# Performance work log

Measured on AMD Instinct MI355X. Metric: run time of the kernel, lower is better.

Reference implementation:

```python
import jax, jax.numpy as jnp
import numpy as np

NBINS = 256

def _rescale_0_1(img):
    return (img + 1.0) * (127.0 / 255.0)

def _rescale_back(img):
    return img * (255.0 / 127.0) - 1.0

def _rgb_to_yuv_y(img):
    # tf.image.rgb_to_yuv luma coefficients; only Y channel is used downstream
    return img[..., 0] * 0.299 + img[..., 1] * 0.587 + img[..., 2] * 0.114

def _equalize_histogram(image):
    # tf.histogram_fixed_width over [0,1] with 256 bins (values clipped to range)
    idx = jnp.clip((image * NBINS).astype(jnp.int32), 0, NBINS - 1)
    hist = jnp.zeros((NBINS,), jnp.int32).at[idx.reshape(-1)].add(1)
    cdf = jnp.cumsum(hist)
    cdf_min = jnp.min(cdf)
    pix_cnt = image.shape[0] * image.shape[1]
    return (cdf - cdf_min).astype(jnp.float32) / jnp.float32(pix_cnt - 1)

def _interpolate(dx, dy, x):
    # brute-force searchsorted substitute: first index where dx - x > 0
    del_vals = dx[jnp.newaxis, :] - x[:, jnp.newaxis]          # [N, 256]
    ind_1 = jnp.argmax(jnp.sign(del_vals), axis=1)             # first positive
    ind_0 = jnp.clip(ind_1 - 1, 0, NBINS - 1)
    dx0, dx1 = dx[ind_0], dx[ind_1]
    dy0, dy1 = dy[ind_0], dy[ind_1]
    denom = dx1 - dx0
    safe_denom = jnp.where(denom == 0, jnp.float32(1.0), denom)
    interp = dy0 + (dy1 - dy0) * (x - dx0) / safe_denom
    return jnp.where(x <= dx[0], dy[0], jnp.where(x >= dx[-1], dy[-1], interp))

def setup_inputs() -> dict:
    key = jax.random.key(0)
    k1, k2 = jax.random.split(key)
    H, W = 1024, 1024
    src = jax.random.uniform(k1, (H, W, 3), jnp.float32, minval=-1.0, maxval=1.0)
    tgt = jax.random.uniform(k2, (H, W, 3), jnp.float32, minval=-1.0, maxval=1.0)
    return {"src": src, "tgt": tgt}

def reference(src, tgt):
    src = _rescale_0_1(src)
    tgt = _rescale_0_1(tgt)
    tgt_y = _rgb_to_yuv_y(tgt)
    h, w = src.shape[0], src.shape[1]
    floating_space = jnp.clip(jnp.arange(0.0, 1.00001, 1.0 / 255.0, dtype=jnp.float32), 0.0, 1.0)
    source = src[:, :, 0]
    cdfsrc = _equalize_histogram(source)
    cdftgt = _equalize_histogram(tgt_y)
    pxmap = _interpolate(cdftgt, floating_space, cdfsrc)
    pxmap = _interpolate(floating_space, pxmap, source.reshape(h * w))
    pxmap = pxmap.reshape(h, w, 1)
    res = jnp.clip(pxmap, 0.0, 1.0)
    return _rescale_back(res)
```

## Files before the change

kernel.cpp:

```cpp
#include <hip/hip_runtime.h>

#define NBINS 256
#define HBLK 512

__device__ __forceinline__ float fs_val(int j) {
    const float c = (float)(1.0 / 255.0);
    float v = (float)j * c;
    return v > 1.0f ? 1.0f : v;
}

__device__ __forceinline__ int bin_of(float s) {
    int i = (int)(s * 256.0f);
    i = i < 0 ? 0 : i;
    i = i > NBINS - 1 ? NBINS - 1 : i;
    return i;
}

__global__ void hm_hist(const float* __restrict__ src,
                        const float* __restrict__ tgt,
                        int* __restrict__ partS, int* __restrict__ partT,
                        int nquad) {
    __shared__ int hs[NBINS];
    __shared__ int ht[NBINS];
    for (int i = threadIdx.x; i < NBINS; i += blockDim.x) { hs[i] = 0; ht[i] = 0; }
    __syncthreads();

    const float c1 = (float)(127.0 / 255.0);
    int tid = blockIdx.x * blockDim.x + threadIdx.x;
    int stride = gridDim.x * blockDim.x;

    for (int q = tid; q < nquad; q += stride) {
        const float4* s4 = (const float4*)(src + 12 * (size_t)q);
        float4 a = s4[0], b = s4[1], c = s4[2];
        float p0 = (a.x + 1.0f) * c1;
        float p1 = (a.w + 1.0f) * c1;
        float p2 = (b.z + 1.0f) * c1;
        float p3 = (c.y + 1.0f) * c1;
        atomicAdd(&hs[bin_of(p0)], 1);
        atomicAdd(&hs[bin_of(p1)], 1);
        atomicAdd(&hs[bin_of(p2)], 1);
        atomicAdd(&hs[bin_of(p3)], 1);

        const float4* t4 = (const float4*)(tgt + 12 * (size_t)q);
        float4 ta = t4[0], tb = t4[1], tc = t4[2];
        {
            float r = (ta.x + 1.0f) * c1, g = (ta.y + 1.0f) * c1, bb = (ta.z + 1.0f) * c1;
            atomicAdd(&ht[bin_of(r * 0.299f + g * 0.587f + bb * 0.114f)], 1);
        }
        {
            float r = (ta.w + 1.0f) * c1, g = (tb.x + 1.0f) * c1, bb = (tb.y + 1.0f) * c1;
            atomicAdd(&ht[bin_of(r * 0.299f + g * 0.587f + bb * 0.114f)], 1);
        }
        {
            float r = (tb.z + 1.0f) * c1, g = (tb.w + 1.0f) * c1, bb = (tc.x + 1.0f) * c1;
            atomicAdd(&ht[bin_of(r * 0.299f + g * 0.587f + bb * 0.114f)], 1);
        }
        {
            float r = (tc.y + 1.0f) * c1, g = (tc.z + 1.0f) * c1, bb = (tc.w + 1.0f) * c1;
            atomicAdd(&ht[bin_of(r * 0.299f + g * 0.587f + bb * 0.114f)], 1);
        }
    }
    __syncthreads();
    for (int i = threadIdx.x; i < NBINS; i += blockDim.x) {
        partS[(size_t)blockIdx.x * NBINS + i] = hs[i];
        partT[(size_t)blockIdx.x * NBINS + i] = ht[i];
    }
}

__global__ void __launch_bounds__(1024)
hm_cdf_map(const int* __restrict__ partS,
           const int* __restrict__ partT,
           float* __restrict__ pxmap, int npix) {
    __shared__ int sS[NBINS];
    __shared__ int sT[NBINS];
    __shared__ float cdfT[NBINS];
    int t = threadIdx.x;
    int bin = t & (NBINS - 1);
    int split = t >> 8;

    if (t < NBINS) { sS[t] = 0; sT[t] = 0; }
    __syncthreads();

    int accS = 0, accT = 0;
    for (int b = split; b < HBLK; b += 4) {
        accS += partS[(size_t)b * NBINS + bin];
        accT += partT[(size_t)b * NBINS + bin];
    }
    atomicAdd(&sS[bin], accS);
    atomicAdd(&sT[bin], accT);
    __syncthreads();

    for (int off = 1; off < NBINS; off <<= 1) {
        int vS = 0, vT = 0, aS = 0, aT = 0;
        if (t < NBINS) {
            vS = sS[t]; vT = sT[t];
            if (t >= off) { aS = sS[t - off]; aT = sT[t - off]; }
        }
        __syncthreads();
        if (t < NBINS) { sS[t] = vS + aS; sT[t] = vT + aT; }
        __syncthreads();
    }

    if (t < NBINS) {
        int minS = sS[0], minT = sT[0];
        float denomN = (float)(npix - 1);
        float xS = (float)(sS[t] - minS) / denomN;
        cdfT[t] = (float)(sT[t] - minT) / denomN;
        __syncthreads();

        float res;
        if (xS <= cdfT[0]) {
            res = fs_val(0);
        } else if (xS >= cdfT[NBINS - 1]) {
            res = fs_val(NBINS - 1);
        } else {
            int lo = 0, hi = NBINS - 1;
            while (hi - lo > 1) {
                int mid = (lo + hi) >> 1;
                if (cdfT[mid] > xS) hi = mid; else lo = mid;
            }
            int j1 = hi, j0 = hi - 1;
            float dx0 = cdfT[j0], dx1 = cdfT[j1];
            float dy0 = fs_val(j0), dy1 = fs_val(j1);
            res = dy0 + (dy1 - dy0) * (xS - dx0) / (dx1 - dx0);
        }
        pxmap[t] = res;
    } else {
        __syncthreads();
    }
}

__global__ void hm_apply(const float* __restrict__ src,
                         const float* __restrict__ pxmap,
                         float* __restrict__ out, int nquad) {
    __shared__ float pm[NBINS];
    for (int i = threadIdx.x; i < NBINS; i += blockDim.x) pm[i] = pxmap[i];
    __syncthreads();

    const float c1 = (float)(127.0 / 255.0);
    const float c2 = (float)(255.0 / 127.0);
    int tid = blockIdx.x * blockDim.x + threadIdx.x;
    int stride = gridDim.x * blockDim.x;

    for (int q = tid; q < nquad; q += stride) {
        const float4* s4 = (const float4*)(src + 12 * (size_t)q);
        float4 a = s4[0], b = s4[1], c = s4[2];
        float xv[4] = {a.x, a.w, b.z, c.y};
        float ov[4];
        #pragma unroll
        for (int k = 0; k < 4; ++k) {
            float x = (xv[k] + 1.0f) * c1;
            float r;
            if (x <= 0.0f) {
                r = pm[0];
            } else if (x >= 1.0f) {
                r = pm[NBINS - 1];
            } else {
                int g = (int)(x * 255.0f) + 1;
                g = g < 1 ? 1 : (g > NBINS - 1 ? NBINS - 1 : g);
                while (g < NBINS - 1 && fs_val(g) <= x) ++g;
                while (g > 1 && fs_val(g - 1) > x) --g;
                int j1 = g, j0 = g - 1;
                float dx0 = fs_val(j0), dx1 = fs_val(j1);
                r = pm[j0] + (pm[j1] - pm[j0]) * (x - dx0) / (dx1 - dx0);
            }
            r = r < 0.0f ? 0.0f : (r > 1.0f ? 1.0f : r);
            ov[k] = r * c2 - 1.0f;
        }
        float4 o;
        o.x = ov[0]; o.y = ov[1]; o.z = ov[2]; o.w = ov[3];
        ((float4*)out)[q] = o;
    }
}

extern "C" void kernel_launch(void* const* d_in, const int* in_sizes, int n_in,
                              void* d_out, int out_size, void* d_ws, size_t ws_size,
                              hipStream_t stream) {
    const float* src = (const float*)d_in[0];
    const float* tgt = (const float*)d_in[1];
    float* out = (float*)d_out;

    int npix = out_size;
    int nquad = npix >> 2;

    int* partS = (int*)d_ws;
    int* partT = partS + (size_t)HBLK * NBINS;
    float* pxmap = (float*)(partT + (size_t)HBLK * NBINS);

    hm_hist<<<HBLK, 256, 0, stream>>>(src, tgt, partS, partT, nquad);
    hm_cdf_map<<<1, 1024, 0, stream>>>(partS, partT, pxmap, npix);
    hm_apply<<<(nquad + 255) / 256, 256, 0, stream>>>(src, pxmap, out, nquad);
}
```

Before: 89.12 us.

## Fuse histogram, CDF mapping and apply into one cooperative kernel

Replaces the three-kernel pipeline with a single cooperative kernel that uses grid-wide syncs. Per-block histograms are merged with global atomics instead of partial buffers plus a one-block reduce kernel. Every block then redundantly computes the scan and lookup table in shared memory before applying the map. This removes two launches and the serial single-block reduction, at the cost of grid.sync overhead, global atomic contention, and a fixed 512-block grid for the apply phase.

```diff
diff --git a/kernel.cpp b/kernel.cpp
--- a/kernel.cpp
+++ b/kernel.cpp
@@ -1,7 +1,11 @@
 #include <hip/hip_runtime.h>
+#include <hip/hip_cooperative_groups.h>
+
+namespace cg = cooperative_groups;
 
 #define NBINS 256
-#define HBLK 512
+#define GBLK  512
+#define TPB   256
 
 __device__ __forceinline__ float fs_val(int j) {
     const float c = (float)(1.0 / 255.0);
@@ -16,30 +20,36 @@
     return i;
 }
 
-__global__ void hm_hist(const float* __restrict__ src,
-                        const float* __restrict__ tgt,
-                        int* __restrict__ partS, int* __restrict__ partT,
-                        int nquad) {
-    __shared__ int hs[NBINS];
-    __shared__ int ht[NBINS];
-    for (int i = threadIdx.x; i < NBINS; i += blockDim.x) { hs[i] = 0; ht[i] = 0; }
-    __syncthreads();
+__global__ void __launch_bounds__(TPB, 2)
+hm_all(const float* __restrict__ src, const float* __restrict__ tgt,
+       int* __restrict__ hist ,
+       float* __restrict__ out, int nquad)
+{
+    cg::grid_group grid = cg::this_grid();
 
+    __shared__ int   hs[NBINS];
+    __shared__ int   ht[NBINS];
+    __shared__ float cdfT[NBINS];
+    __shared__ float pm[NBINS];
+
+    const int t    = threadIdx.x;
+    const int gtid = blockIdx.x * TPB + t;
+    const int nth  = GBLK * TPB;
     const float c1 = (float)(127.0 / 255.0);
-    int tid = blockIdx.x * blockDim.x + threadIdx.x;
-    int stride = gridDim.x * blockDim.x;
 
-    for (int q = tid; q < nquad; q += stride) {
+    if (gtid < 2 * NBINS) {
+        __hip_atomic_store(&hist[gtid], 0, __ATOMIC_RELAXED, __HIP_MEMORY_SCOPE_AGENT);
+    }
+    hs[t] = 0; ht[t] = 0;
+    grid.sync();
+
+    for (int q = gtid; q < nquad; q += nth) {
         const float4* s4 = (const float4*)(src + 12 * (size_t)q);
         float4 a = s4[0], b = s4[1], c = s4[2];
-        float p0 = (a.x + 1.0f) * c1;
-        float p1 = (a.w + 1.0f) * c1;
-        float p2 = (b.z + 1.0f) * c1;
-        float p3 = (c.y + 1.0f) * c1;
-        atomicAdd(&hs[bin_of(p0)], 1);
-        atomicAdd(&hs[bin_of(p1)], 1);
-        atomicAdd(&hs[bin_of(p2)], 1);
-        atomicAdd(&hs[bin_of(p3)], 1);
+        atomicAdd(&hs[bin_of((a.x + 1.0f) * c1)], 1);
+        atomicAdd(&hs[bin_of((a.w + 1.0f) * c1)], 1);
+        atomicAdd(&hs[bin_of((b.z + 1.0f) * c1)], 1);
+        atomicAdd(&hs[bin_of((c.y + 1.0f) * c1)], 1);
 
         const float4* t4 = (const float4*)(tgt + 12 * (size_t)q);
         float4 ta = t4[0], tb = t4[1], tc = t4[2];
@@ -61,51 +71,26 @@
         }
     }
     __syncthreads();
-    for (int i = threadIdx.x; i < NBINS; i += blockDim.x) {
-        partS[(size_t)blockIdx.x * NBINS + i] = hs[i];
-        partT[(size_t)blockIdx.x * NBINS + i] = ht[i];
-    }
-}
+    atomicAdd(&hist[t], hs[t]);
+    atomicAdd(&hist[NBINS + t], ht[t]);
+    grid.sync();
 
-__global__ void __launch_bounds__(1024)
-hm_cdf_map(const int* __restrict__ partS,
-           const int* __restrict__ partT,
-           float* __restrict__ pxmap, int npix) {
-    __shared__ int sS[NBINS];
-    __shared__ int sT[NBINS];
-    __shared__ float cdfT[NBINS];
-    int t = threadIdx.x;
-    int bin = t & (NBINS - 1);
-    int split = t >> 8;
-
-    if (t < NBINS) { sS[t] = 0; sT[t] = 0; }
-    __syncthreads();
-
-    int accS = 0, accT = 0;
-    for (int b = split; b < HBLK; b += 4) {
-        accS += partS[(size_t)b * NBINS + bin];
-        accT += partT[(size_t)b * NBINS + bin];
-    }
-    atomicAdd(&sS[bin], accS);
-    atomicAdd(&sT[bin], accT);
-    __syncthreads();
-
-    for (int off = 1; off < NBINS; off <<= 1) {
-        int vS = 0, vT = 0, aS = 0, aT = 0;
-        if (t < NBINS) {
-            vS = sS[t]; vT = sT[t];
-            if (t >= off) { aS = sS[t - off]; aT = sT[t - off]; }
+    {
+        int vS = __hip_atomic_load(&hist[t],         __ATOMIC_ACQUIRE, __HIP_MEMORY_SCOPE_AGENT);
+        int vT = __hip_atomic_load(&hist[NBINS + t], __ATOMIC_ACQUIRE, __HIP_MEMORY_SCOPE_AGENT);
+        hs[t] = vS; ht[t] = vT;
+        __syncthreads();
+        for (int off = 1; off < NBINS; off <<= 1) {
+            int aS = (t >= off) ? hs[t - off] : 0;
+            int aT = (t >= off) ? ht[t - off] : 0;
+            __syncthreads();
+            hs[t] += aS; ht[t] += aT;
+            __syncthreads();
         }
-        __syncthreads();
-        if (t < NBINS) { sS[t] = vS + aS; sT[t] = vT + aT; }
-        __syncthreads();
-    }
-
-    if (t < NBINS) {
-        int minS = sS[0], minT = sT[0];
-        float denomN = (float)(npix - 1);
-        float xS = (float)(sS[t] - minS) / denomN;
-        cdfT[t] = (float)(sT[t] - minT) / denomN;
+        int minS = hs[0], minT = ht[0];
+        float denomN = (float)(4 * nquad - 1);
+        float xS = (float)(hs[t] - minS) / denomN;
+        cdfT[t]  = (float)(ht[t] - minT) / denomN;
         __syncthreads();
 
         float res;
@@ -124,25 +109,12 @@
             float dy0 = fs_val(j0), dy1 = fs_val(j1);
             res = dy0 + (dy1 - dy0) * (xS - dx0) / (dx1 - dx0);
         }
-        pxmap[t] = res;
-    } else {
+        pm[t] = res;
         __syncthreads();
     }
-}
 
-__global__ void hm_apply(const float* __restrict__ src,
-                         const float* __restrict__ pxmap,
-                         float* __restrict__ out, int nquad) {
-    __shared__ float pm[NBINS];
-    for (int i = threadIdx.x; i < NBINS; i += blockDim.x) pm[i] = pxmap[i];
-    __syncthreads();
-
-    const float c1 = (float)(127.0 / 255.0);
     const float c2 = (float)(255.0 / 127.0);
-    int tid = blockIdx.x * blockDim.x + threadIdx.x;
-    int stride = gridDim.x * blockDim.x;
-
-    for (int q = tid; q < nquad; q += stride) {
+    for (int q = gtid; q < nquad; q += nth) {
         const float4* s4 = (const float4*)(src + 12 * (size_t)q);
         float4 a = s4[0], b = s4[1], c = s4[2];
         float xv[4] = {a.x, a.w, b.z, c.y};
@@ -180,14 +152,9 @@
     const float* tgt = (const float*)d_in[1];
     float* out = (float*)d_out;
 
-    int npix = out_size;
-    int nquad = npix >> 2;
+    int nquad = out_size >> 2;
+    int* hist = (int*)d_ws;
 
-    int* partS = (int*)d_ws;
-    int* partT = partS + (size_t)HBLK * NBINS;
-    float* pxmap = (float*)(partT + (size_t)HBLK * NBINS);
-
-    hm_hist<<<HBLK, 256, 0, stream>>>(src, tgt, partS, partT, nquad);
-    hm_cdf_map<<<1, 1024, 0, stream>>>(partS, partT, pxmap, npix);
-    hm_apply<<<(nquad + 255) / 256, 256, 0, stream>>>(src, pxmap, out, nquad);
+    void* kargs[] = { (void*)&src, (void*)&tgt, (void*)&hist, (void*)&out, (void*)&nquad };
+    hipLaunchCooperativeKernel((void*)hm_all, dim3(GBLK), dim3(TPB), kargs, 0, stream);
 }
```

After: 217.8 us. 2.44x slower.
